# Performance work log

Measured on AMD Instinct MI355X. Metric: run time of the kernel, lower is better.

## Reference

```python
import jax, jax.numpy as jnp
import numpy as np

N_NODES = 100000
N_EDGES = 1600000
DIM = 128
NUM_FEATURES = 128
NUM_LAYERS = 3


def _linear_params(key, fan_in, fan_out):
    kw, kb = jax.random.split(key)
    bound = 1.0 / np.sqrt(fan_in)
    W = jax.random.uniform(kw, (fan_in, fan_out), jnp.float32, -bound, bound)
    b = jax.random.uniform(kb, (fan_out,), jnp.float32, -bound, bound)
    return W, b


def setup_inputs() -> dict:
    key = jax.random.key(0)
    ks = jax.random.split(key, 16)
    x = jax.random.normal(ks[0], (N_NODES, NUM_FEATURES), jnp.float32)
    edge_index = jax.random.randint(ks[1], (2, N_EDGES), 0, N_NODES, jnp.int64)
    batch = jnp.zeros((N_NODES,), jnp.int64)
    inp = {"x": x, "edge_index": edge_index, "batch": batch}
    # GINConv MLPs: layer i has Linear(in, DIM) -> ReLU -> Linear(DIM, DIM)
    for i in range(NUM_LAYERS):
        fan_in = NUM_FEATURES if i == 0 else DIM
        W1, b1 = _linear_params(ks[2 + 2 * i], fan_in, DIM)
        W2, b2 = _linear_params(ks[3 + 2 * i], DIM, DIM)
        inp[f"W1_{i}"], inp[f"b1_{i}"] = W1, b1
        inp[f"W2_{i}"], inp[f"b2_{i}"] = W2, b2
    # readout == 'concat' -> final Linear(DIM * NUM_LAYERS, 1)
    Wm, bm = _linear_params(ks[10], DIM * NUM_LAYERS, 1)
    inp["Wm"], inp["bm"] = Wm, bm
    return inp


def _gin_layer(x, W1, b1, W2, b2, src, dst):
    # GINConv with eps=0: MLP(x_i + sum_{j->i} x_j)
    agg = jax.ops.segment_sum(x[src], dst, num_segments=N_NODES)  # [N, d]
    h = agg + x
    h = jnp.maximum(h @ W1 + b1, 0.0)
    return h @ W2 + b2


def _forward(x, params, Wm, bm, src, dst):
    xs = []
    for i in range(NUM_LAYERS):
        W1, b1, W2, b2 = params[i]
        x = _gin_layer(x, W1, b1, W2, b2, src, dst)
        if i != NUM_LAYERS - 1:
            x = jnp.maximum(x, 0.0)
        xs.append(x)
    node_prob = jnp.concatenate(xs, axis=1)  # readout == 'concat'
    return jax.nn.sigmoid(node_prob @ Wm + bm)


def reference(x, edge_index, batch,
              W1_0, b1_0, W2_0, b2_0,
              W1_1, b1_1, W2_1, b2_1,
              W1_2, b1_2, W2_2, b2_2,
              Wm, bm):
    src, dst = edge_index[0], edge_index[1]
    params = [(W1_0, b1_0, W2_0, b2_0),
              (W1_1, b1_1, W2_1, b2_1),
              (W1_2, b1_2, W2_2, b2_2)]
    return _forward(x, params, Wm, bm, src, dst)
```

## Files before the change

kernel.cpp:

```cpp
#include <hip/hip_runtime.h>
#include <hip/hip_bf16.h>

#define N_NODES 100000
#define N_EDGES 1600000
#define DIM 128

#define NB    782
#define NPB   128
#define BSTR  2944
#define CHUNK 4096

typedef __attribute__((ext_vector_type(8))) short bf16x8;
typedef __attribute__((ext_vector_type(4))) float f32x4;

__device__ __forceinline__ short f2bf(float f) {
    union { float f; unsigned u; } v; v.f = f;
    unsigned r = (v.u + 0x7fff + ((v.u >> 16) & 1)) >> 16;
    return (short)r;
}
__device__ __forceinline__ unsigned pk(float lo, float hi) {
    return (unsigned)(unsigned short)f2bf(lo) | ((unsigned)(unsigned short)f2bf(hi) << 16);
}
__device__ __forceinline__ float bl(unsigned p) {
    union { unsigned u; float f; } v; v.u = p << 16; return v.f;
}
__device__ __forceinline__ float bh(unsigned p) {
    union { unsigned u; float f; } v; v.u = p & 0xffff0000u; return v.f;
}

__global__ __launch_bounds__(256) void prep_kernel(
    const float* __restrict__ x, unsigned short* __restrict__ xb,
    const float* __restrict__ W0, const float* __restrict__ W1,
    const float* __restrict__ W2, const float* __restrict__ W3,
    const float* __restrict__ W4, const float* __restrict__ W5,
    unsigned short* __restrict__ T)
{
    int b = blockIdx.x, t = threadIdx.x;
    if (b < 6250) {
        long long i = (long long)b * 256 + t;
        const float4* p = (const float4*)(x + i * 8);
        float4 a = p[0], c = p[1];
        uint4 o;
        o.x = pk(a.x, a.y); o.y = pk(a.z, a.w);
        o.z = pk(c.x, c.y); o.w = pk(c.z, c.w);
        *(uint4*)(xb + i * 8) = o;
    } else {
        int idx = (b - 6250) * 256 + t;
        int m = idx >> 14, rem = idx & 16383;
        int n = rem >> 7, k = rem & 127;
        const float* W = (m == 0) ? W0 : (m == 1) ? W1 : (m == 2) ? W2
                       : (m == 3) ? W3 : (m == 4) ? W4 : W5;
        T[(size_t)m * DIM * DIM + n * DIM + k] = (unsigned short)f2bf(W[k * DIM + n]);
    }
}

__global__ __launch_bounds__(256) void bucketA_kernel(
    const int* __restrict__ src, const int* __restrict__ dst,
    int* __restrict__ gcur, unsigned* __restrict__ barr)
{
    __shared__ int cnt[NB];
    __shared__ int base[NB];
    const int t = threadIdx.x;
    const long long e0 = (long long)blockIdx.x * CHUNK;
    const int ecnt = (int)((e0 + CHUNK <= N_EDGES) ? CHUNK : (N_EDGES - e0));

    for (int i = t; i < NB; i += 256) cnt[i] = 0;
    __syncthreads();
    for (int i = t; i < ecnt; i += 256)
        atomicAdd(&cnt[dst[e0 + i] >> 7], 1);
    __syncthreads();
    for (int i = t; i < NB; i += 256) {
        int c = cnt[i];
        base[i] = c ? atomicAdd(&gcur[i], c) : 0;
        cnt[i] = 0;
    }
    __syncthreads();
    for (int i = t; i < ecnt; i += 256) {
        int d = dst[e0 + i], s = src[e0 + i];
        int bk = d >> 7;
        int r = atomicAdd(&cnt[bk], 1);
        barr[(long long)bk * BSTR + base[bk] + r] =
            (unsigned)s | ((unsigned)(d & 127) << 20);
    }
}

__global__ __launch_bounds__(64) void scanb_kernel(
    const int* __restrict__ gcur, int* __restrict__ cbase)
{
    int lane = threadIdx.x;
    int carry = 0;
    for (int b0 = 0; b0 < NB; b0 += 64) {
        int v = (b0 + lane < NB) ? gcur[b0 + lane] : 0;
        int s = v;
#pragma unroll
        for (int ofs = 1; ofs < 64; ofs <<= 1) {
            int u = __shfl_up(s, ofs);
            if (lane >= ofs) s += u;
        }
        if (b0 + lane < NB) cbase[b0 + lane] = carry + s - v;
        carry += __shfl(s, 63);
    }
    if (lane == 0) cbase[NB] = carry;
}

__global__ __launch_bounds__(256) void bucketB_kernel(
    const unsigned* __restrict__ barr, const int* __restrict__ gcur,
    const int* __restrict__ cbase, int* __restrict__ off, int* __restrict__ csr)
{
    __shared__ int cnt[NPB];
    __shared__ int cur[NPB];
    __shared__ int sbase, sn;
    const int b = blockIdx.x, t = threadIdx.x;
    if (t < NPB) cnt[t] = 0;
    if (t == 0) { sbase = cbase[b]; sn = gcur[b]; }
    __syncthreads();
    const int n = sn;
    const unsigned* be = barr + (long long)b * BSTR;
    for (int i = t; i < n; i += 256)
        atomicAdd(&cnt[(be[i] >> 20) & 127], 1);
    __syncthreads();
    if (t < 64) {
        int carry = 0;
#pragma unroll
        for (int k = 0; k < 2; ++k) {
            int idx = k * 64 + t;
            int v = cnt[idx], s = v;
#pragma unroll
            for (int ofs = 1; ofs < 64; ofs <<= 1) {
                int u = __shfl_up(s, ofs);
                if (t >= ofs) s += u;
            }
            cur[idx] = carry + s - v;
            carry += __shfl(s, 63);
        }
    }
    __syncthreads();
    if (t < NPB) {
        int node = b * NPB + t;
        if (node < N_NODES) off[node] = sbase + cur[t];
    }
    if (b == NB - 1 && t == 0) off[N_NODES] = cbase[NB];
    __syncthreads();
    for (int i = t; i < n; i += 256) {
        unsigned r = be[i];
        int j = (r >> 20) & 127;
        int p = atomicAdd(&cur[j], 1);
        csr[sbase + p] = (int)(r & 0xFFFFF);
    }
}

__global__ __launch_bounds__(256) void gather_kernel(
    const unsigned short* __restrict__ xb,
    const int* __restrict__ off, const int* __restrict__ csr,
    unsigned short* __restrict__ ab)
{
    long long gt = (long long)blockIdx.x * 256 + threadIdx.x;
    int node = (int)(gt >> 6);
    int lane = (int)(gt & 63);
    if (node >= N_NODES) return;
    const int g = lane >> 4, l4 = lane & 15;
    const int beg = off[node], end = off[node + 1];
    float acc[8] = {0.f, 0.f, 0.f, 0.f, 0.f, 0.f, 0.f, 0.f};
    int j = beg + g;
    for (; j + 4 < end; j += 8) {
        int s0 = csr[j], s1 = csr[j + 4];
        uint4 v0 = *(const uint4*)(xb + (long long)s0 * DIM + l4 * 8);
        uint4 v1 = *(const uint4*)(xb + (long long)s1 * DIM + l4 * 8);
        acc[0] += bl(v0.x) + bl(v1.x); acc[1] += bh(v0.x) + bh(v1.x);
        acc[2] += bl(v0.y) + bl(v1.y); acc[3] += bh(v0.y) + bh(v1.y);
        acc[4] += bl(v0.z) + bl(v1.z); acc[5] += bh(v0.z) + bh(v1.z);
        acc[6] += bl(v0.w) + bl(v1.w); acc[7] += bh(v0.w) + bh(v1.w);
    }
    for (; j < end; j += 4) {
        int s = csr[j];
        uint4 v = *(const uint4*)(xb + (long long)s * DIM + l4 * 8);
        acc[0] += bl(v.x); acc[1] += bh(v.x);
        acc[2] += bl(v.y); acc[3] += bh(v.y);
        acc[4] += bl(v.z); acc[5] += bh(v.z);
        acc[6] += bl(v.w); acc[7] += bh(v.w);
    }
#pragma unroll
    for (int k = 0; k < 8; ++k) {
        acc[k] += __shfl_xor(acc[k], 16);
        acc[k] += __shfl_xor(acc[k], 32);
    }
    if (g == 0) {
        uint4 sv = *(const uint4*)(xb + (long long)node * DIM + l4 * 8);
        acc[0] += bl(sv.x); acc[1] += bh(sv.x);
        acc[2] += bl(sv.y); acc[3] += bh(sv.y);
        acc[4] += bl(sv.z); acc[5] += bh(sv.z);
        acc[6] += bl(sv.w); acc[7] += bh(sv.w);
        uint4 o;
        o.x = pk(acc[0], acc[1]); o.y = pk(acc[2], acc[3]);
        o.z = pk(acc[4], acc[5]); o.w = pk(acc[6], acc[7]);
        *(uint4*)(ab + (long long)node * DIM + l4 * 8) = o;
    }
}

__global__ __launch_bounds__(256) void gin_mlp_kernel(
    const unsigned short* __restrict__ ab,
    const unsigned short* __restrict__ Wt1, const float* __restrict__ b1,
    const unsigned short* __restrict__ Wt2, const float* __restrict__ b2,
    unsigned short* __restrict__ outb, int relu_out, int N)
{
    __shared__ short As[128][136];
    __shared__ short Hs[128][136];

    const int t = threadIdx.x;
    const long long row0 = (long long)blockIdx.x * 128;

    {
        const int r = t >> 1, c0 = (t & 1) * 64;
        const long long gr = row0 + r;
        if (gr < N) {
            const unsigned short* pa = ab + gr * DIM + c0;
#pragma unroll
            for (int v = 0; v < 8; ++v)
                *(uint4*)&As[r][c0 + v * 8] = *(const uint4*)(pa + v * 8);
        } else {
#pragma unroll
            for (int v = 0; v < 8; ++v)
                *(uint4*)&As[r][c0 + v * 8] = make_uint4(0, 0, 0, 0);
        }
    }
    __syncthreads();

    const int w = t >> 6, lane = t & 63;
    const int wr = (w >> 1) * 64, wc = (w & 1) * 64;
    const int fr = lane & 15, kg = lane >> 4;

    f32x4 acc[4][4] = {};
#pragma unroll
    for (int k0 = 0; k0 < 128; k0 += 32) {
        bf16x8 a[4], b[4];
#pragma unroll
        for (int mi = 0; mi < 4; ++mi)
            a[mi] = *(const bf16x8*)&As[wr + mi * 16 + fr][k0 + kg * 8];
#pragma unroll
        for (int ni = 0; ni < 4; ++ni)
            b[ni] = *(const bf16x8*)(Wt1 + (long long)(wc + ni * 16 + fr) * DIM + k0 + kg * 8);
#pragma unroll
        for (int mi = 0; mi < 4; ++mi)
#pragma unroll
            for (int ni = 0; ni < 4; ++ni)
                acc[mi][ni] = __builtin_amdgcn_mfma_f32_16x16x32_bf16(
                    a[mi], b[ni], acc[mi][ni], 0, 0, 0);
    }

    {
        float bia[4];
#pragma unroll
        for (int ni = 0; ni < 4; ++ni) bia[ni] = b1[wc + ni * 16 + fr];
#pragma unroll
        for (int mi = 0; mi < 4; ++mi)
#pragma unroll
            for (int ni = 0; ni < 4; ++ni)
#pragma unroll
                for (int j = 0; j < 4; ++j) {
                    int r = wr + mi * 16 + kg * 4 + j;
                    int c = wc + ni * 16 + fr;
                    float hv = acc[mi][ni][j] + bia[ni];
                    Hs[r][c] = f2bf(hv > 0.f ? hv : 0.f);
                }
    }
    __syncthreads();

    f32x4 acc2[4][4] = {};
#pragma unroll
    for (int k0 = 0; k0 < 128; k0 += 32) {
        bf16x8 a[4], b[4];
#pragma unroll
        for (int mi = 0; mi < 4; ++mi)
            a[mi] = *(const bf16x8*)&Hs[wr + mi * 16 + fr][k0 + kg * 8];
#pragma unroll
        for (int ni = 0; ni < 4; ++ni)
            b[ni] = *(const bf16x8*)(Wt2 + (long long)(wc + ni * 16 + fr) * DIM + k0 + kg * 8);
#pragma unroll
        for (int mi = 0; mi < 4; ++mi)
#pragma unroll
            for (int ni = 0; ni < 4; ++ni)
                acc2[mi][ni] = __builtin_amdgcn_mfma_f32_16x16x32_bf16(
                    a[mi], b[ni], acc2[mi][ni], 0, 0, 0);
    }
    __syncthreads();

    {
        float bia[4];
#pragma unroll
        for (int ni = 0; ni < 4; ++ni) bia[ni] = b2[wc + ni * 16 + fr];
#pragma unroll
        for (int mi = 0; mi < 4; ++mi)
#pragma unroll
            for (int ni = 0; ni < 4; ++ni)
#pragma unroll
                for (int j = 0; j < 4; ++j) {
                    int r = wr + mi * 16 + kg * 4 + j;
                    int c = wc + ni * 16 + fr;
                    float v2 = acc2[mi][ni][j] + bia[ni];
                    if (relu_out && v2 < 0.f) v2 = 0.f;
                    Hs[r][c] = f2bf(v2);
                }
    }
    __syncthreads();

    {
        const int r = t >> 1, c0 = (t & 1) * 64;
        const long long gr = row0 + r;
        if (gr < N) {
            unsigned short* po = outb + gr * DIM + c0;
#pragma unroll
            for (int v = 0; v < 8; ++v)
                *(uint4*)(po + v * 8) = *(const uint4*)&Hs[r][c0 + v * 8];
        }
    }
}

__global__ __launch_bounds__(256) void readout_kernel(
    const unsigned short* __restrict__ hb,
    const float* __restrict__ Wm, const float* __restrict__ bm,
    float* __restrict__ out, int N)
{
    long long gt = (long long)blockIdx.x * 256 + threadIdx.x;
    int node = (int)(gt >> 6);
    int lane = (int)(gt & 63);
    if (node >= N) return;
    float s = 0.f;
#pragma unroll
    for (int g = 0; g < 3; ++g) {
        unsigned v = *(const unsigned*)(hb + ((long long)g * N + node) * DIM + lane * 2);
        float2 wv = *(const float2*)(Wm + g * DIM + lane * 2);
        s += bl(v) * wv.x + bh(v) * wv.y;
    }
#pragma unroll
    for (int ofs = 32; ofs > 0; ofs >>= 1) s += __shfl_down(s, ofs);
    if (lane == 0) out[node] = 1.f / (1.f + __expf(-(s + bm[0])));
}

extern "C" void kernel_launch(void* const* d_in, const int* in_sizes, int n_in,
                              void* d_out, int out_size, void* d_ws, size_t ws_size,
                              hipStream_t stream)
{
    const float* x  = (const float*)d_in[0];
    const int*   ei = (const int*)d_in[1];
    const int*   src = ei;
    const int*   dst = ei + N_EDGES;
    const float* W1[3] = { (const float*)d_in[3], (const float*)d_in[7],  (const float*)d_in[11] };
    const float* b1[3] = { (const float*)d_in[4], (const float*)d_in[8],  (const float*)d_in[12] };
    const float* W2[3] = { (const float*)d_in[5], (const float*)d_in[9],  (const float*)d_in[13] };
    const float* b2[3] = { (const float*)d_in[6], (const float*)d_in[10], (const float*)d_in[14] };
    const float* Wm = (const float*)d_in[15];
    const float* bm = (const float*)d_in[16];
    float* out = (float*)d_out;

    char* p = (char*)d_ws;
    unsigned short* xb = (unsigned short*)p; p += (size_t)N_NODES * DIM * 2;
    unsigned short* ab = (unsigned short*)p; p += (size_t)N_NODES * DIM * 2;
    unsigned short* hb = (unsigned short*)p; p += (size_t)3 * N_NODES * DIM * 2;
    unsigned short* Wt = (unsigned short*)p; p += (size_t)6 * DIM * DIM * 2;
    int* off  = (int*)p;     p += (size_t)(N_NODES + 1) * sizeof(int);
    int* csr  = (int*)p;     p += (size_t)N_EDGES * sizeof(int);
    int* gcur = (int*)p;     p += (size_t)NB * sizeof(int);
    int* cbase = (int*)p;    p += (size_t)(NB + 1) * sizeof(int);
    unsigned* barr = (unsigned*)p; p += (size_t)NB * BSTR * sizeof(unsigned);

    const int mlp_blocks  = (N_NODES + 127) / 128;
    const int wave_blocks = (N_NODES * 64 + 255) / 256;
    const int pa_blocks   = (N_EDGES + CHUNK - 1) / CHUNK;

    hipMemsetAsync(gcur, 0, (size_t)NB * sizeof(int), stream);
    bucketA_kernel<<<pa_blocks, 256, 0, stream>>>(src, dst, gcur, barr);
    scanb_kernel<<<1, 64, 0, stream>>>(gcur, cbase);
    bucketB_kernel<<<NB, 256, 0, stream>>>(barr, gcur, cbase, off, csr);

    prep_kernel<<<6250 + 384, 256, 0, stream>>>(
        x, xb, W1[0], W2[0], W1[1], W2[1], W1[2], W2[2], Wt);

    const unsigned short* xin_b = xb;
    for (int layer = 0; layer < 3; ++layer) {
        gather_kernel<<<wave_blocks, 256, 0, stream>>>(xin_b, off, csr, ab);
        gin_mlp_kernel<<<mlp_blocks, 256, 0, stream>>>(
            ab, Wt + (size_t)(2 * layer) * DIM * DIM, b1[layer],
            Wt + (size_t)(2 * layer + 1) * DIM * DIM, b2[layer],
            hb + (size_t)layer * N_NODES * DIM, (layer != 2) ? 1 : 0, N_NODES);
        xin_b = hb + (size_t)layer * N_NODES * DIM;
    }
    readout_kernel<<<wave_blocks, 256, 0, stream>>>(hb, Wm, bm, out, N_NODES);
}
```

Measured before the change: 487.3 us.

## Fuse readout into last-layer MLP, unroll gather by four, share one LDS tile

The sigmoid readout moves into the third-layer MLP kernel, which reads the two earlier layer outputs from global memory and the final layer from shared memory. This removes the separate readout launch and the write and re-read of the last layer's activations. The gather loop now issues four neighbor loads per iteration instead of two to raise memory-level parallelism. The two LDS tiles are merged into one, which needs an extra barrier and puts a serial 64-element dot product per thread in the epilogue.

```diff
diff --git a/kernel.cpp b/kernel.cpp
--- a/kernel.cpp
+++ b/kernel.cpp
@@ -26,6 +26,9 @@
 }
 __device__ __forceinline__ float bh(unsigned p) {
     union { unsigned u; float f; } v; v.u = p & 0xffff0000u; return v.f;
+}
+__device__ __forceinline__ float bfs(short s) {
+    union { unsigned u; float f; } v; v.u = ((unsigned)(unsigned short)s) << 16; return v.f;
 }
 
 __global__ __launch_bounds__(256) void prep_kernel(
@@ -162,14 +165,20 @@
     const int beg = off[node], end = off[node + 1];
     float acc[8] = {0.f, 0.f, 0.f, 0.f, 0.f, 0.f, 0.f, 0.f};
     int j = beg + g;
-    for (; j + 4 < end; j += 8) {
-        int s0 = csr[j], s1 = csr[j + 4];
+    for (; j + 12 < end; j += 16) {
+        int s0 = csr[j], s1 = csr[j + 4], s2 = csr[j + 8], s3 = csr[j + 12];
         uint4 v0 = *(const uint4*)(xb + (long long)s0 * DIM + l4 * 8);
         uint4 v1 = *(const uint4*)(xb + (long long)s1 * DIM + l4 * 8);
-        acc[0] += bl(v0.x) + bl(v1.x); acc[1] += bh(v0.x) + bh(v1.x);
-        acc[2] += bl(v0.y) + bl(v1.y); acc[3] += bh(v0.y) + bh(v1.y);
-        acc[4] += bl(v0.z) + bl(v1.z); acc[5] += bh(v0.z) + bh(v1.z);
-        acc[6] += bl(v0.w) + bl(v1.w); acc[7] += bh(v0.w) + bh(v1.w);
+        uint4 v2 = *(const uint4*)(xb + (long long)s2 * DIM + l4 * 8);
+        uint4 v3 = *(const uint4*)(xb + (long long)s3 * DIM + l4 * 8);
+        acc[0] += (bl(v0.x) + bl(v1.x)) + (bl(v2.x) + bl(v3.x));
+        acc[1] += (bh(v0.x) + bh(v1.x)) + (bh(v2.x) + bh(v3.x));
+        acc[2] += (bl(v0.y) + bl(v1.y)) + (bl(v2.y) + bl(v3.y));
+        acc[3] += (bh(v0.y) + bh(v1.y)) + (bh(v2.y) + bh(v3.y));
+        acc[4] += (bl(v0.z) + bl(v1.z)) + (bl(v2.z) + bl(v3.z));
+        acc[5] += (bh(v0.z) + bh(v1.z)) + (bh(v2.z) + bh(v3.z));
+        acc[6] += (bl(v0.w) + bl(v1.w)) + (bl(v2.w) + bl(v3.w));
+        acc[7] += (bh(v0.w) + bh(v1.w)) + (bh(v2.w) + bh(v3.w));
     }
     for (; j < end; j += 4) {
         int s = csr[j];
@@ -201,27 +210,27 @@
     const unsigned short* __restrict__ ab,
     const unsigned short* __restrict__ Wt1, const float* __restrict__ b1,
     const unsigned short* __restrict__ Wt2, const float* __restrict__ b2,
-    unsigned short* __restrict__ outb, int relu_out, int N)
-{
-    __shared__ short As[128][136];
-    __shared__ short Hs[128][136];
+    unsigned short* __restrict__ outb,
+    const unsigned short* __restrict__ hb0, const unsigned short* __restrict__ hb1,
+    const float* __restrict__ Wm, const float* __restrict__ bm,
+    float* __restrict__ out, int mode, int N)
+{
+    __shared__ short S[128][136];
 
     const int t = threadIdx.x;
     const long long row0 = (long long)blockIdx.x * 128;
-
-    {
-        const int r = t >> 1, c0 = (t & 1) * 64;
-        const long long gr = row0 + r;
-        if (gr < N) {
-            const unsigned short* pa = ab + gr * DIM + c0;
-#pragma unroll
-            for (int v = 0; v < 8; ++v)
-                *(uint4*)&As[r][c0 + v * 8] = *(const uint4*)(pa + v * 8);
-        } else {
-#pragma unroll
-            for (int v = 0; v < 8; ++v)
-                *(uint4*)&As[r][c0 + v * 8] = make_uint4(0, 0, 0, 0);
-        }
+    const int r = t >> 1, half = t & 1, c0 = half * 64;
+    const long long gr = row0 + r;
+
+    if (gr < N) {
+        const unsigned short* pa = ab + gr * DIM + c0;
+#pragma unroll
+        for (int v = 0; v < 8; ++v)
+            *(uint4*)&S[r][c0 + v * 8] = *(const uint4*)(pa + v * 8);
+    } else {
+#pragma unroll
+        for (int v = 0; v < 8; ++v)
+            *(uint4*)&S[r][c0 + v * 8] = make_uint4(0, 0, 0, 0);
     }
     __syncthreads();
 
@@ -235,7 +244,7 @@
         bf16x8 a[4], b[4];
 #pragma unroll
         for (int mi = 0; mi < 4; ++mi)
-            a[mi] = *(const bf16x8*)&As[wr + mi * 16 + fr][k0 + kg * 8];
+            a[mi] = *(const bf16x8*)&S[wr + mi * 16 + fr][k0 + kg * 8];
 #pragma unroll
         for (int ni = 0; ni < 4; ++ni)
             b[ni] = *(const bf16x8*)(Wt1 + (long long)(wc + ni * 16 + fr) * DIM + k0 + kg * 8);
@@ -246,6 +255,7 @@
                 acc[mi][ni] = __builtin_amdgcn_mfma_f32_16x16x32_bf16(
                     a[mi], b[ni], acc[mi][ni], 0, 0, 0);
     }
+    __syncthreads();
 
     {
         float bia[4];
@@ -257,10 +267,10 @@
             for (int ni = 0; ni < 4; ++ni)
 #pragma unroll
                 for (int j = 0; j < 4; ++j) {
-                    int r = wr + mi * 16 + kg * 4 + j;
-                    int c = wc + ni * 16 + fr;
+                    int rr = wr + mi * 16 + kg * 4 + j;
+                    int cc = wc + ni * 16 + fr;
                     float hv = acc[mi][ni][j] + bia[ni];
-                    Hs[r][c] = f2bf(hv > 0.f ? hv : 0.f);
+                    S[rr][cc] = f2bf(hv > 0.f ? hv : 0.f);
                 }
     }
     __syncthreads();
@@ -271,7 +281,7 @@
         bf16x8 a[4], b[4];
 #pragma unroll
         for (int mi = 0; mi < 4; ++mi)
-            a[mi] = *(const bf16x8*)&Hs[wr + mi * 16 + fr][k0 + kg * 8];
+            a[mi] = *(const bf16x8*)&S[wr + mi * 16 + fr][k0 + kg * 8];
 #pragma unroll
         for (int ni = 0; ni < 4; ++ni)
             b[ni] = *(const bf16x8*)(Wt2 + (long long)(wc + ni * 16 + fr) * DIM + k0 + kg * 8);
@@ -294,46 +304,51 @@
             for (int ni = 0; ni < 4; ++ni)
 #pragma unroll
                 for (int j = 0; j < 4; ++j) {
-                    int r = wr + mi * 16 + kg * 4 + j;
-                    int c = wc + ni * 16 + fr;
+                    int rr = wr + mi * 16 + kg * 4 + j;
+                    int cc = wc + ni * 16 + fr;
                     float v2 = acc2[mi][ni][j] + bia[ni];
-                    if (relu_out && v2 < 0.f) v2 = 0.f;
-                    Hs[r][c] = f2bf(v2);
+                    if (mode == 1 && v2 < 0.f) v2 = 0.f;
+                    S[rr][cc] = f2bf(v2);
                 }
     }
     __syncthreads();
 
-    {
-        const int r = t >> 1, c0 = (t & 1) * 64;
-        const long long gr = row0 + r;
+    if (mode == 1) {
         if (gr < N) {
             unsigned short* po = outb + gr * DIM + c0;
 #pragma unroll
             for (int v = 0; v < 8; ++v)
-                *(uint4*)(po + v * 8) = *(const uint4*)&Hs[r][c0 + v * 8];
+                *(uint4*)(po + v * 8) = *(const uint4*)&S[r][c0 + v * 8];
         }
-    }
-}
-
-__global__ __launch_bounds__(256) void readout_kernel(
-    const unsigned short* __restrict__ hb,
-    const float* __restrict__ Wm, const float* __restrict__ bm,
-    float* __restrict__ out, int N)
-{
-    long long gt = (long long)blockIdx.x * 256 + threadIdx.x;
-    int node = (int)(gt >> 6);
-    int lane = (int)(gt & 63);
-    if (node >= N) return;
-    float s = 0.f;
-#pragma unroll
-    for (int g = 0; g < 3; ++g) {
-        unsigned v = *(const unsigned*)(hb + ((long long)g * N + node) * DIM + lane * 2);
-        float2 wv = *(const float2*)(Wm + g * DIM + lane * 2);
-        s += bl(v) * wv.x + bh(v) * wv.y;
-    }
-#pragma unroll
-    for (int ofs = 32; ofs > 0; ofs >>= 1) s += __shfl_down(s, ofs);
-    if (lane == 0) out[node] = 1.f / (1.f + __expf(-(s + bm[0])));
+    } else {
+        float s = 0.f;
+        if (gr < N) {
+            const unsigned short* p0 = hb0 + gr * DIM + c0;
+            const unsigned short* p1 = hb1 + gr * DIM + c0;
+#pragma unroll
+            for (int v = 0; v < 8; ++v) {
+                uint4 u0 = *(const uint4*)(p0 + v * 8);
+                uint4 u1 = *(const uint4*)(p1 + v * 8);
+                const float* wm0 = Wm + c0 + v * 8;
+                const float* wm1 = Wm + 128 + c0 + v * 8;
+                s += bl(u0.x) * wm0[0] + bh(u0.x) * wm0[1]
+                   + bl(u0.y) * wm0[2] + bh(u0.y) * wm0[3]
+                   + bl(u0.z) * wm0[4] + bh(u0.z) * wm0[5]
+                   + bl(u0.w) * wm0[6] + bh(u0.w) * wm0[7];
+                s += bl(u1.x) * wm1[0] + bh(u1.x) * wm1[1]
+                   + bl(u1.y) * wm1[2] + bh(u1.y) * wm1[3]
+                   + bl(u1.z) * wm1[4] + bh(u1.z) * wm1[5]
+                   + bl(u1.w) * wm1[6] + bh(u1.w) * wm1[7];
+            }
+            const float* wm2 = Wm + 256 + c0;
+#pragma unroll
+            for (int c = 0; c < 64; ++c)
+                s += bfs(S[r][c0 + c]) * wm2[c];
+        }
+        s += __shfl_xor(s, 1);
+        if (half == 0 && gr < N)
+            out[gr] = 1.f / (1.f + __expf(-(s + bm[0])));
+    }
 }
 
 extern "C" void kernel_launch(void* const* d_in, const int* in_sizes, int n_in,
@@ -355,7 +370,7 @@
     char* p = (char*)d_ws;
     unsigned short* xb = (unsigned short*)p; p += (size_t)N_NODES * DIM * 2;
     unsigned short* ab = (unsigned short*)p; p += (size_t)N_NODES * DIM * 2;
-    unsigned short* hb = (unsigned short*)p; p += (size_t)3 * N_NODES * DIM * 2;
+    unsigned short* hb = (unsigned short*)p; p += (size_t)2 * N_NODES * DIM * 2;
     unsigned short* Wt = (unsigned short*)p; p += (size_t)6 * DIM * DIM * 2;
     int* off  = (int*)p;     p += (size_t)(N_NODES + 1) * sizeof(int);
     int* csr  = (int*)p;     p += (size_t)N_EDGES * sizeof(int);
@@ -375,14 +390,16 @@
     prep_kernel<<<6250 + 384, 256, 0, stream>>>(
         x, xb, W1[0], W2[0], W1[1], W2[1], W1[2], W2[2], Wt);
 
+    unsigned short* hbuf[2] = { hb, hb + (size_t)N_NODES * DIM };
     const unsigned short* xin_b = xb;
     for (int layer = 0; layer < 3; ++layer) {
         gather_kernel<<<wave_blocks, 256, 0, stream>>>(xin_b, off, csr, ab);
+        int mode = (layer != 2) ? 1 : 2;
         gin_mlp_kernel<<<mlp_blocks, 256, 0, stream>>>(
             ab, Wt + (size_t)(2 * layer) * DIM * DIM, b1[layer],
             Wt + (size_t)(2 * layer + 1) * DIM * DIM, b2[layer],
-            hb + (size_t)layer * N_NODES * DIM, (layer != 2) ? 1 : 0, N_NODES);
-        xin_b = hb + (size_t)layer * N_NODES * DIM;
-    }
-    readout_kernel<<<wave_blocks, 256, 0, stream>>>(hb, Wm, bm, out, N_NODES);
-}
+            (mode == 1) ? hbuf[layer] : (unsigned short*)nullptr,
+            hbuf[0], hbuf[1], Wm, bm, out, mode, N_NODES);
+        if (mode == 1) xin_b = hbuf[layer];
+    }
+}
```

Result: no change. 478.7 us (-1.8%).
